# Performance work log

Measured on AMD Instinct MI355X. Metric: run time of the kernel, lower is better.

## Reference

```python
import jax, jax.numpy as jnp
import numpy as np

B, S, EMB, H = 4, 1024, 1024, 16
HD = EMB // H          # head_dim = 64
MAXP = 512             # RelativePositionalEncoder default max_position


def setup_inputs() -> dict:
    key = jax.random.key(0)
    ks = jax.random.split(key, 13)
    s = 1.0 / np.sqrt(EMB)  # xavier-ish scale keeps softmax logits sane
    return {
        "query": jax.random.normal(ks[0], (B, S, EMB), jnp.float32),
        "key": jax.random.normal(ks[1], (B, S, EMB), jnp.float32),
        "value": jax.random.normal(ks[2], (B, S, EMB), jnp.float32),
        "Wq": jax.random.normal(ks[3], (EMB, EMB), jnp.float32) * s,
        "bq": jnp.zeros((EMB,), jnp.float32),
        "Wk": jax.random.normal(ks[4], (EMB, EMB), jnp.float32) * s,
        "bk": jnp.zeros((EMB,), jnp.float32),
        "Wv": jax.random.normal(ks[5], (EMB, EMB), jnp.float32) * s,
        "bv": jnp.zeros((EMB,), jnp.float32),
        "Wo": jax.random.normal(ks[6], (EMB, EMB), jnp.float32) * s,
        "bo": jnp.zeros((EMB,), jnp.float32),
        "rel_k": jax.random.normal(ks[7], (2 * MAXP + 1, HD), jnp.float32) * 0.05,
        "rel_v": jax.random.normal(ks[8], (2 * MAXP + 1, HD), jnp.float32) * 0.05,
    }


def _split_heads(x):
    # [B,S,E] -> [B,S,H,HD] -> [B,H,S,HD] -> [B*H,S,HD]
    return x.reshape(B, S, H, HD).transpose(0, 2, 1, 3).reshape(B * H, S, HD)


def reference(query, key, value, Wq, bq, Wk, bk, Wv, bv, Wo, bo, rel_k, rel_v):
    scale = jnp.sqrt(jnp.asarray(HD, query.dtype))
    q = _split_heads(query @ Wq + bq)
    k = _split_heads(key @ Wk + bk)
    v = _split_heads(value @ Wv + bv)
    # relative position lookup tables: [Sq, Sk, HD]
    rp = jnp.clip(jnp.arange(S)[None, :] - jnp.arange(S)[:, None], -MAXP, MAXP) + MAXP
    a_key = rel_k[rp]
    a_value = rel_v[rp]
    qk = jnp.einsum('bqd,bkd->bqk', q, k)              # [B*H,S,S]
    rel_qk = jnp.einsum('bqd,qkd->bqk', q, a_key)      # relative score term
    attn = jax.nn.softmax((qk + rel_qk) / scale, axis=-1)
    out = jnp.einsum('bqk,bkd->bqd', attn, v) + jnp.einsum('bqk,qkd->bqd', attn, a_value)
    # faithful to original's view(num_heads, batch, -1, head_dim) then concat reshape
    out = out.reshape(H, B, S, HD).transpose(0, 2, 1, 3).reshape(B, S, H * HD)
    out = out @ Wo + bo
    return (out, attn)
```

## Files before the change

### kernel.cpp

```cpp
#include <hip/hip_runtime.h>


using s16x8 = __attribute__((ext_vector_type(8))) short;
using f32x4 = __attribute__((ext_vector_type(4))) float;

#define MFMA16 __builtin_amdgcn_mfma_f32_16x16x32_bf16

__device__ __forceinline__ float bf2f(unsigned short u) {
  union { unsigned int u; float f; } v; v.u = ((unsigned int)u) << 16; return v.f;
}
__device__ __forceinline__ unsigned short f2bf(float f) {
  union { float f; unsigned int u; } v; v.f = f;
  unsigned int r = (v.u + 0x7FFFu + ((v.u >> 16) & 1u)) >> 16;
  return (unsigned short)r;
}

__global__ void k_cvt_bf16(const float* __restrict__ in, unsigned short* __restrict__ out, int n) {
  int i = (blockIdx.x * 256 + threadIdx.x) * 8;
  if (i >= n) return;
  float4 a = *(const float4*)(in + i);
  float4 b = *(const float4*)(in + i + 4);
  s16x8 o;
  o[0] = (short)f2bf(a.x); o[1] = (short)f2bf(a.y); o[2] = (short)f2bf(a.z); o[3] = (short)f2bf(a.w);
  o[4] = (short)f2bf(b.x); o[5] = (short)f2bf(b.y); o[6] = (short)f2bf(b.z); o[7] = (short)f2bf(b.w);
  *(s16x8*)(out + i) = o;
}

__global__ void k_tr1024(const float* __restrict__ W, unsigned short* __restrict__ Wt) {
  __shared__ float t[32][33];
  int tx = threadIdx.x, ty = threadIdx.y;
  int n0 = blockIdx.x * 32, k0 = blockIdx.y * 32;
#pragma unroll
  for (int r = 0; r < 4; ++r)
    t[ty * 4 + r][tx] = W[(size_t)(k0 + ty * 4 + r) * 1024 + n0 + tx];
  __syncthreads();
#pragma unroll
  for (int r = 0; r < 4; ++r)
    Wt[(size_t)(n0 + ty * 4 + r) * 1024 + k0 + tx] = f2bf(t[tx][ty * 4 + r]);
}

__global__ void k_relprep(const float* __restrict__ rk, const float* __restrict__ rv,
                          unsigned short* __restrict__ relkb, unsigned short* __restrict__ rvTb) {
  int b = blockIdx.x;
  if (b < 33) {
    int i = (b * 256 + threadIdx.x) * 8;
    if (i < 65600) {
      float4 a = *(const float4*)(rk + i);
      float4 c = *(const float4*)(rk + i + 4);
      s16x8 o;
      o[0] = (short)f2bf(a.x); o[1] = (short)f2bf(a.y); o[2] = (short)f2bf(a.z); o[3] = (short)f2bf(a.w);
      o[4] = (short)f2bf(c.x); o[5] = (short)f2bf(c.y); o[6] = (short)f2bf(c.z); o[7] = (short)f2bf(c.w);
      *(s16x8*)(relkb + i) = o;
    }
  } else {
    int i = (b - 33) * 256 + threadIdx.x;
    if (i < 65600) {
      int p = i >> 6, d = i & 63;
      rvTb[d * 1040 + p] = f2bf(rv[i]);
    }
  }
}

__global__ __launch_bounds__(256)
void k_trV(const unsigned short* __restrict__ v, unsigned short* __restrict__ vt) {
  __shared__ unsigned short T[64][72];
  const int tid = threadIdx.x;
  const int bh = blockIdx.x >> 4;
  const int s0 = (blockIdx.x & 15) << 6;
  const int r = tid >> 2, cb = (tid & 3) << 4;
  const unsigned short* src = v + ((size_t)bh << 16) + (size_t)(s0 + r) * 64 + cb;
  *(s16x8*)&T[r][cb] = *(const s16x8*)src;
  *(s16x8*)&T[r][cb + 8] = *(const s16x8*)(src + 8);
  __syncthreads();
  unsigned short* dst = vt + ((size_t)bh << 16) + (size_t)r * 1024 + s0 + cb;
  s16x8 o0, o1;
#pragma unroll
  for (int e = 0; e < 8; ++e) o0[e] = T[cb + e][r];
#pragma unroll
  for (int e = 0; e < 8; ++e) o1[e] = T[cb + 8 + e][r];
  *(s16x8*)dst = o0;
  *(s16x8*)(dst + 8) = o1;
}

template <int MODE>
__global__ __launch_bounds__(256, 2)
void k_gemm(const unsigned short* __restrict__ A, const unsigned short* __restrict__ BT,
            const float* __restrict__ bias, void* __restrict__ Cout) {
  __shared__ alignas(16) unsigned short aT[2][4096];
  __shared__ alignas(16) unsigned short bT[2][2048];
  const int tid = threadIdx.x;
  const int lane = tid & 63;
  const int l15 = lane & 15, lhi = lane >> 4;
  const int w = tid >> 6;
  const int wr = w * 32;
  const int brow = blockIdx.y * 128, bcol = blockIdx.x * 64;
  f32x4 acc[2][4] = {};

#define STAGE(buf, kt) do {                                                              \
    int k0s = (kt) * 32;                                                                 \
    {                                                                                    \
      int c = tid;                                                                       \
      int row = c >> 2, k8 = (c & 3) * 8;                                                \
      __builtin_amdgcn_global_load_lds(                                                  \
        (const __attribute__((address_space(1))) void*)(A + (size_t)(brow + row) * 1024 + k0s + k8), \
        (__attribute__((address_space(3))) void*)(&aT[buf][c * 8]), 16, 0, 0);           \
      __builtin_amdgcn_global_load_lds(                                                  \
        (const __attribute__((address_space(1))) void*)(BT + (size_t)(bcol + row) * 1024 + k0s + k8),\
        (__attribute__((address_space(3))) void*)(&bT[buf][c * 8]), 16, 0, 0);           \
    }                                                                                    \
    {                                                                                    \
      int c = tid + 256;                                                                 \
      int row = c >> 2, k8 = (c & 3) * 8;                                                \
      __builtin_amdgcn_global_load_lds(                                                  \
        (const __attribute__((address_space(1))) void*)(A + (size_t)(brow + row) * 1024 + k0s + k8), \
        (__attribute__((address_space(3))) void*)(&aT[buf][c * 8]), 16, 0, 0);           \
    }                                                                                    \
  } while (0)

  int cur = 0;
  STAGE(0, 0);
  for (int kt = 0; kt < 32; ++kt) {
    __syncthreads();
    if (kt + 1 < 32) STAGE(cur ^ 1, kt + 1);
    s16x8 af[2], bfv[4];
#pragma unroll
    for (int m = 0; m < 2; ++m)
      af[m] = *(const s16x8*)&aT[cur][(wr + m * 16 + l15) * 32 + lhi * 8];
#pragma unroll
    for (int n = 0; n < 4; ++n)
      bfv[n] = *(const s16x8*)&bT[cur][(n * 16 + l15) * 32 + lhi * 8];
#pragma unroll
    for (int m = 0; m < 2; ++m)
#pragma unroll
      for (int n = 0; n < 4; ++n)
        acc[m][n] = MFMA16(af[m], bfv[n], acc[m][n], 0, 0, 0);
    __syncthreads();
    cur ^= 1;
  }
#undef STAGE

#pragma unroll
  for (int m = 0; m < 2; ++m) {
#pragma unroll
    for (int n = 0; n < 4; ++n) {
      int col = bcol + n * 16 + l15;
      float bs = bias[col];
#pragma unroll
      for (int j = 0; j < 4; ++j) {
        int r = brow + wr + m * 16 + lhi * 4 + j;
        float v = acc[m][n][j] + bs;
        if (MODE == 0) {
          int b = r >> 10, s = r & 1023, h = col >> 6, d = col & 63;
          ((unsigned short*)Cout)[(((size_t)((b << 4) + h) * 1024 + s) << 6) + d] = f2bf(v);
        } else {
          ((float*)Cout)[(size_t)r * 1024 + col] = v;
        }
      }
    }
  }
}

#define RPW 1032
#define PWP 520

__global__ __launch_bounds__(256, 3)
void k_attn(const unsigned short* __restrict__ qb, const unsigned short* __restrict__ kbm,
            const unsigned short* __restrict__ vT, const unsigned short* __restrict__ relk,
            const unsigned short* __restrict__ rvT, float* __restrict__ attn_out,
            unsigned short* __restrict__ xscr) {
  __shared__ alignas(16) unsigned short pbuf[16 * RPW];
  __shared__ alignas(16) unsigned short pw[16 * PWP];
  __shared__ float red[4][16];
  __shared__ float izS[16], plS[16], phS[16];

  const int tid = threadIdx.x;
  const int lane = tid & 63;
  const int w = tid >> 6;
  const int l15 = lane & 15, lhi = lane >> 4;
  const int orig = ((blockIdx.x & 7) << 9) | (blockIdx.x >> 3);
  const int bh = orig >> 6;
  const int q0 = (orig & 63) << 4;

  const unsigned short* Qh = qb + ((size_t)bh << 16);
  const unsigned short* Kh = kbm + ((size_t)bh << 16);
  const unsigned short* Vth = vT + ((size_t)bh << 16);

  const unsigned short* qp = Qh + (size_t)(q0 + l15) * 64 + lhi * 8;
  s16x8 qa0 = *(const s16x8*)qp;
  s16x8 qa1 = *(const s16x8*)(qp + 32);

  float zp[4] = {0.f, 0.f, 0.f, 0.f};
  for (int k0 = w * 16; k0 < 1024; k0 += 64) {
    const unsigned short* kp = Kh + (size_t)(k0 + l15) * 64 + lhi * 8;
    s16x8 kf0 = *(const s16x8*)kp;
    s16x8 kf1 = *(const s16x8*)(kp + 32);
    const int jb = k0 - q0 - 15;
    int p0 = jb + l15;      p0 = (p0 < -512 ? -512 : (p0 > 512 ? 512 : p0)) + 512;
    int p1 = jb + l15 + 16; p1 = (p1 < -512 ? -512 : (p1 > 512 ? 512 : p1)) + 512;
    const unsigned short* r0p = relk + (size_t)p0 * 64 + lhi * 8;
    const unsigned short* r1p = relk + (size_t)p1 * 64 + lhi * 8;
    s16x8 ra0 = *(const s16x8*)r0p, ra0h = *(const s16x8*)(r0p + 32);
    s16x8 ra1 = *(const s16x8*)r1p, ra1h = *(const s16x8*)(r1p + 32);
    f32x4 c = {0.f, 0.f, 0.f, 0.f};
    f32x4 w0 = {0.f, 0.f, 0.f, 0.f}, w1 = {0.f, 0.f, 0.f, 0.f};
    __builtin_amdgcn_s_setprio(1);
    c = MFMA16(qa0, kf0, c, 0, 0, 0);
    c = MFMA16(qa1, kf1, c, 0, 0, 0);
    w0 = MFMA16(qa0, ra0, w0, 0, 0, 0);  w0 = MFMA16(qa1, ra0h, w0, 0, 0, 0);
    w1 = MFMA16(qa0, ra1, w1, 0, 0, 0);  w1 = MFMA16(qa1, ra1h, w1, 0, 0, 0);
    __builtin_amdgcn_s_setprio(0);
#pragma unroll
    for (int j = 0; j < 4; ++j) {
      int qi = lhi * 4 + j;
      int ts = l15 - qi + 15;
      int sl = (lane & 48) | (ts & 15);
      float a0 = __shfl(w0[j], sl, 64);
      float a1 = __shfl(w1[j], sl, 64);
      float rel = (ts & 16) ? a1 : a0;
      float e = __expf((c[j] + rel) * 0.125f);
      zp[j] += e;
      pbuf[qi * RPW + k0 + l15] = f2bf(e);
    }
  }
#pragma unroll
  for (int off = 1; off < 16; off <<= 1)
#pragma unroll
    for (int j = 0; j < 4; ++j) zp[j] += __shfl_xor(zp[j], off, 64);
  if (l15 == 0) {
#pragma unroll
    for (int j = 0; j < 4; ++j) red[w][lhi * 4 + j] = zp[j];
  }
  __syncthreads();
  if (tid < 16)
    izS[tid] = 1.0f / (red[0][tid] + red[1][tid] + red[2][tid] + red[3][tid]);

  {
    const int qi = tid >> 4, tq = tid & 15;
    const int qa = q0 + qi;
    int lo, hi;
    const bool isPh = (qa < 512);
    if (isPh) { lo = qa + 512; hi = 1024; }
    else      { lo = 0;        hi = qa - 511; }
    float s = 0.f;
    const unsigned short* srow = pbuf + qi * RPW;
    const int kb0 = lo & ~7;
    for (int k8 = kb0 + tq * 8; k8 < hi; k8 += 128) {
      s16x8 v8 = *(const s16x8*)&srow[k8];
#pragma unroll
      for (int e = 0; e < 8; ++e) {
        int k = k8 + e;
        s += (k >= lo && k < hi) ? bf2f((unsigned short)v8[e]) : 0.f;
      }
    }
#pragma unroll
    for (int off = 1; off < 16; off <<= 1) s += __shfl_xor(s, off, 64);
    if (tq == 0) { plS[qi] = isPh ? 0.f : s; phS[qi] = isPh ? s : 0.f; }
  }
  __syncthreads();

  {
    float* ao = attn_out + ((size_t)bh << 20) + ((size_t)q0 << 10);
#pragma unroll
    for (int n = 0; n < 16; ++n) {
      float iz = izS[n];
      union { unsigned int u[2]; } pv;
      *(uint2*)pv.u = *(const uint2*)&pbuf[n * RPW + tid * 4];
      union { unsigned int u; float f; } b0, b1, b2, b3;
      b0.u = pv.u[0] << 16; b1.u = pv.u[0] & 0xFFFF0000u;
      b2.u = pv.u[1] << 16; b3.u = pv.u[1] & 0xFFFF0000u;
      f32x4 o;
      o[0] = b0.f * iz; o[1] = b1.f * iz; o[2] = b2.f * iz; o[3] = b3.f * iz;
      __builtin_nontemporal_store(o, (f32x4*)(ao + (n << 10) + tid * 4));
    }
  }

  f32x4 acc = {0.f, 0.f, 0.f, 0.f};
  const int d0w = w << 4;
  const unsigned short* vrow = Vth + (size_t)(d0w + l15) * 1024 + lhi * 8;
#pragma unroll 8
  for (int kc = 0; kc < 1024; kc += 32) {
    s16x8 pa = *(const s16x8*)&pbuf[l15 * RPW + kc + lhi * 8];
    s16x8 vf = *(const s16x8*)(vrow + kc);
    acc = MFMA16(pa, vf, acc, 0, 0, 0);
  }

  const unsigned short* rrow = rvT + (size_t)(d0w + l15) * 1040 + lhi * 8;
  {
    const int sqi = tid >> 4, stq = tid & 15;
    const int ssh = sqi & 7, shs = ssh >> 1;
    const bool sodd = (ssh & 1) != 0;
    unsigned short* drow = pw + sqi * PWP;
    const unsigned short* srow = pbuf + sqi * RPW;
    for (int ph = 0; ph < 2; ++ph) {
      __syncthreads();
      const int base = q0 + sqi + (ph ? 0 : -512);
      for (int t = stq; t < 64; t += 16) {
        const int kw0 = base + t * 8;
        s16x8 o;
        if (kw0 >= 0 && kw0 + 8 <= 1024) {
          const int A = kw0 - ssh;
          union { s16x8 v; unsigned int u[4]; } a0, a1, ov;
          a0.v = *(const s16x8*)&srow[A];
          a1.v = *(const s16x8*)&srow[A + 8];
          unsigned int wd[8];
#pragma unroll
          for (int j2 = 0; j2 < 4; ++j2) { wd[j2] = a0.u[j2]; wd[4 + j2] = a1.u[j2]; }
          unsigned int v7[7];
#pragma unroll
          for (int j2 = 0; j2 < 7; ++j2) {
            unsigned int sf = (wd[j2] >> 16) | (wd[j2 + 1] << 16);
            v7[j2] = sodd ? sf : wd[j2];
          }
#pragma unroll
          for (int j2 = 0; j2 < 4; ++j2) {
            unsigned int t0 = (shs & 1) ? v7[j2 + 1] : v7[j2];
            unsigned int t1 = (shs & 1) ? v7[j2 + 3] : v7[j2 + 2];
            ov.u[j2] = (shs & 2) ? t1 : t0;
          }
          o = ov.v;
        } else if (kw0 + 8 <= 0 || kw0 >= 1024) {
          o = (s16x8){0, 0, 0, 0, 0, 0, 0, 0};
        } else {
#pragma unroll
          for (int e = 0; e < 8; ++e) {
            int k = kw0 + e;
            int kc2 = k < 0 ? 0 : (k > 1023 ? 1023 : k);
            unsigned short vv = srow[kc2];
            o[e] = (k >= 0 && k < 1024) ? (short)vv : (short)0;
          }
        }
        *(s16x8*)&drow[t * 8] = o;
        if (ph == 0 && t == 0) drow[0] = f2bf(plS[sqi]);
      }
      __syncthreads();
#pragma unroll 8
      for (int kc = 0; kc < 512; kc += 32) {
        s16x8 pa = *(const s16x8*)&pw[l15 * PWP + kc + lhi * 8];
        s16x8 rb = *(const s16x8*)(rrow + (ph << 9) + kc);
        acc = MFMA16(pa, rb, acc, 0, 0, 0);
      }
    }
  }

  float rv1024 = bf2f(rvT[(size_t)(d0w + l15) * 1040 + 1024]);
  const size_t fb = ((size_t)(bh >> 2) << 18) + ((size_t)(bh & 3) << 6);
#pragma unroll
  for (int j = 0; j < 4; ++j) {
    int qi = lhi * 4 + j;
    float v = (acc[j] + phS[qi] * rv1024) * izS[qi];
    xscr[fb + ((size_t)(q0 + qi) << 8) + d0w + l15] = f2bf(v);
  }
}

extern "C" void kernel_launch(void* const* d_in, const int* in_sizes, int n_in,
                              void* d_out, int out_size, void* d_ws, size_t ws_size,
                              hipStream_t stream) {
  (void)in_sizes; (void)n_in; (void)out_size; (void)ws_size;
  const float* query = (const float*)d_in[0];
  const float* key   = (const float*)d_in[1];
  const float* value = (const float*)d_in[2];
  const float* Wq = (const float*)d_in[3];
  const float* bq = (const float*)d_in[4];
  const float* Wk = (const float*)d_in[5];
  const float* bk = (const float*)d_in[6];
  const float* Wv = (const float*)d_in[7];
  const float* bv = (const float*)d_in[8];
  const float* Wo = (const float*)d_in[9];
  const float* bo = (const float*)d_in[10];
  const float* rel_k = (const float*)d_in[11];
  const float* rel_v = (const float*)d_in[12];

  char* ws = (char*)d_ws;
  const size_t MB = 1024 * 1024;
  unsigned short* qb    = (unsigned short*)(ws);
  unsigned short* kbuf  = (unsigned short*)(ws + 8 * MB);
  unsigned short* vbuf  = (unsigned short*)(ws + 16 * MB);
  unsigned short* tmp16 = (unsigned short*)(ws + 24 * MB);
  unsigned short* wt    = (unsigned short*)(ws + 32 * MB);
  unsigned short* relkb = (unsigned short*)(ws + 34 * MB);
  unsigned short* rvTb  = (unsigned short*)(ws + 34 * MB + 512 * 1024);
  unsigned short* vTb   = tmp16;
  unsigned short* xscr  = vbuf;

  float* out0 = (float*)d_out;
  float* attn_out = out0 + 4194304;

  dim3 trb(32, 8), trg(32, 32);
  dim3 gg(16, 32);

  k_relprep<<<290, 256, 0, stream>>>(rel_k, rel_v, relkb, rvTb);

  k_cvt_bf16<<<2048, 256, 0, stream>>>(query, tmp16, 4194304);
  k_tr1024<<<trg, trb, 0, stream>>>(Wq, wt);
  k_gemm<0><<<gg, 256, 0, stream>>>(tmp16, wt, bq, qb);

  k_cvt_bf16<<<2048, 256, 0, stream>>>(key, tmp16, 4194304);
  k_tr1024<<<trg, trb, 0, stream>>>(Wk, wt);
  k_gemm<0><<<gg, 256, 0, stream>>>(tmp16, wt, bk, kbuf);

  k_cvt_bf16<<<2048, 256, 0, stream>>>(value, tmp16, 4194304);
  k_tr1024<<<trg, trb, 0, stream>>>(Wv, wt);
  k_gemm<0><<<gg, 256, 0, stream>>>(tmp16, wt, bv, vbuf);

  k_trV<<<1024, 256, 0, stream>>>(vbuf, vTb);
  k_tr1024<<<trg, trb, 0, stream>>>(Wo, wt);

  k_attn<<<4096, 256, 0, stream>>>(qb, kbuf, vTb, relkb, rvTb, attn_out, xscr);

  k_gemm<1><<<gg, 256, 0, stream>>>(xscr, wt, bo, out0);
}
```

Before: 395.8 us.

## Precompute relative-key score table per block instead of per-tile MFMAs

Replaces the per-key-tile computation of two relative-key MFMA pairs plus shuffles with a per-half precomputed table of q·rel_k values stored in shared memory. Only the unclipped relative positions need MFMAs, and the clipped boundary values are broadcast. The QK MFMA operands are swapped so each lane holds contiguous keys, which lets it pack four bf16 probabilities into one store. The attention write-out is also widened to 16-byte shared loads. This adds extra barriers and table-building passes in exchange for fewer MFMAs and cross-lane shuffles in the score loop.

```diff
diff --git a/kernel.cpp b/kernel.cpp
--- a/kernel.cpp
+++ b/kernel.cpp
@@ -169,9 +169,10 @@
             const unsigned short* __restrict__ rvT, float* __restrict__ attn_out,
             unsigned short* __restrict__ xscr) {
   __shared__ alignas(16) unsigned short pbuf[16 * RPW];
-  __shared__ alignas(16) unsigned short pw[16 * PWP];
+  __shared__ alignas(16) unsigned short TbPw[16 * PWP];
   __shared__ float red[4][16];
   __shared__ float izS[16], plS[16], phS[16];
+  __shared__ unsigned short bndS[32];
 
   const int tid = threadIdx.x;
   const int lane = tid & 63;
@@ -189,47 +190,89 @@
   s16x8 qa0 = *(const s16x8*)qp;
   s16x8 qa1 = *(const s16x8*)(qp + 32);
 
-  float zp[4] = {0.f, 0.f, 0.f, 0.f};
-  for (int k0 = w * 16; k0 < 1024; k0 += 64) {
-    const unsigned short* kp = Kh + (size_t)(k0 + l15) * 64 + lhi * 8;
-    s16x8 kf0 = *(const s16x8*)kp;
-    s16x8 kf1 = *(const s16x8*)(kp + 32);
-    const int jb = k0 - q0 - 15;
-    int p0 = jb + l15;      p0 = (p0 < -512 ? -512 : (p0 > 512 ? 512 : p0)) + 512;
-    int p1 = jb + l15 + 16; p1 = (p1 < -512 ? -512 : (p1 > 512 ? 512 : p1)) + 512;
-    const unsigned short* r0p = relk + (size_t)p0 * 64 + lhi * 8;
-    const unsigned short* r1p = relk + (size_t)p1 * 64 + lhi * 8;
-    s16x8 ra0 = *(const s16x8*)r0p, ra0h = *(const s16x8*)(r0p + 32);
-    s16x8 ra1 = *(const s16x8*)r1p, ra1h = *(const s16x8*)(r1p + 32);
-    f32x4 c = {0.f, 0.f, 0.f, 0.f};
-    f32x4 w0 = {0.f, 0.f, 0.f, 0.f}, w1 = {0.f, 0.f, 0.f, 0.f};
-    __builtin_amdgcn_s_setprio(1);
-    c = MFMA16(qa0, kf0, c, 0, 0, 0);
-    c = MFMA16(qa1, kf1, c, 0, 0, 0);
-    w0 = MFMA16(qa0, ra0, w0, 0, 0, 0);  w0 = MFMA16(qa1, ra0h, w0, 0, 0, 0);
-    w1 = MFMA16(qa0, ra1, w1, 0, 0, 0);  w1 = MFMA16(qa1, ra1h, w1, 0, 0, 0);
-    __builtin_amdgcn_s_setprio(0);
-#pragma unroll
-    for (int j = 0; j < 4; ++j) {
-      int qi = lhi * 4 + j;
-      int ts = l15 - qi + 15;
-      int sl = (lane & 48) | (ts & 15);
-      float a0 = __shfl(w0[j], sl, 64);
-      float a1 = __shfl(w1[j], sl, 64);
-      float rel = (ts & 16) ? a1 : a0;
-      float e = __expf((c[j] + rel) * 0.125f);
-      zp[j] += e;
-      pbuf[qi * RPW + k0 + l15] = f2bf(e);
-    }
-  }
-#pragma unroll
-  for (int off = 1; off < 16; off <<= 1)
-#pragma unroll
-    for (int j = 0; j < 4; ++j) zp[j] += __shfl_xor(zp[j], off, 64);
-  if (l15 == 0) {
-#pragma unroll
-    for (int j = 0; j < 4; ++j) red[w][lhi * 4 + j] = zp[j];
-  }
+  {
+    int sel = (l15 == 1) ? 1024 : 0;
+    const unsigned short* rp = relk + (size_t)sel * 64 + lhi * 8;
+    s16x8 rb0 = *(const s16x8*)rp;
+    s16x8 rb1 = *(const s16x8*)(rp + 32);
+    f32x4 d = {0.f, 0.f, 0.f, 0.f};
+    d = MFMA16(qa0, rb0, d, 0, 0, 0);
+    d = MFMA16(qa1, rb1, d, 0, 0, 0);
+    if (l15 < 2) {
+#pragma unroll
+      for (int j = 0; j < 4; ++j) bndS[l15 * 16 + lhi * 4 + j] = f2bf(d[j]);
+    }
+  }
+
+  float zp = 0.f;
+  for (int half = 0; half < 2; ++half) {
+    const int khalf = half << 9;
+    __syncthreads();
+
+    for (int i = tid; i < 16 * 64; i += 256) {
+      int row = i >> 6, c8 = (i & 63) << 3;
+      int fl = q0 + row - khalf - 512;
+      unsigned short vlo = bndS[row], vhi = bndS[16 + row];
+      s16x8 o;
+#pragma unroll
+      for (int e = 0; e < 8; ++e) o[e] = (short)((c8 + e < fl) ? vlo : vhi);
+      *(s16x8*)&TbPw[row * PWP + c8] = o;
+    }
+    __syncthreads();
+
+    {
+      int pmin = khalf - q0 + 497;
+      int PT0 = (pmin < 0 ? 0 : pmin) & ~15;
+      int PT1 = khalf - q0 + 1023; if (PT1 > 1024) PT1 = 1024;
+      for (int pt = PT0 + w * 16; pt <= PT1; pt += 64) {
+        int pr = pt + l15; if (pr > 1024) pr = 1024;
+        const unsigned short* rp = relk + (size_t)pr * 64 + lhi * 8;
+        s16x8 rf0 = *(const s16x8*)rp;
+        s16x8 rf1 = *(const s16x8*)(rp + 32);
+        f32x4 d = {0.f, 0.f, 0.f, 0.f};
+        d = MFMA16(qa0, rf0, d, 0, 0, 0);
+        d = MFMA16(qa1, rf1, d, 0, 0, 0);
+#pragma unroll
+        for (int j = 0; j < 4; ++j) {
+          int qi = lhi * 4 + j;
+          int p = pt + l15;
+          int u = p - khalf + q0 + qi - 512;
+          if (p <= 1024 && u >= 0 && u < 512) TbPw[qi * PWP + u] = f2bf(d[j]);
+        }
+      }
+    }
+    __syncthreads();
+
+    for (int n = 0; n < 8; ++n) {
+      const int ktile = khalf + w * 16 + n * 64;
+      const unsigned short* kp = Kh + (size_t)(ktile + l15) * 64 + lhi * 8;
+      s16x8 kf0 = *(const s16x8*)kp;
+      s16x8 kf1 = *(const s16x8*)(kp + 32);
+      f32x4 c = {0.f, 0.f, 0.f, 0.f};
+      __builtin_amdgcn_s_setprio(1);
+      c = MFMA16(kf0, qa0, c, 0, 0, 0);
+      c = MFMA16(kf1, qa1, c, 0, 0, 0);
+      __builtin_amdgcn_s_setprio(0);
+      uint2 tv = *(const uint2*)&TbPw[l15 * PWP + (ktile - khalf) + lhi * 4];
+      float t0 = bf2f((unsigned short)(tv.x & 0xFFFF));
+      float t1 = bf2f((unsigned short)(tv.x >> 16));
+      float t2 = bf2f((unsigned short)(tv.y & 0xFFFF));
+      float t3 = bf2f((unsigned short)(tv.y >> 16));
+      float e0 = __expf((c[0] + t0) * 0.125f);
+      float e1 = __expf((c[1] + t1) * 0.125f);
+      float e2 = __expf((c[2] + t2) * 0.125f);
+      float e3 = __expf((c[3] + t3) * 0.125f);
+      zp += (e0 + e1) + (e2 + e3);
+      uint2 pk;
+      pk.x = (unsigned int)f2bf(e0) | ((unsigned int)f2bf(e1) << 16);
+      pk.y = (unsigned int)f2bf(e2) | ((unsigned int)f2bf(e3) << 16);
+      *(uint2*)&pbuf[l15 * RPW + ktile + lhi * 4] = pk;
+    }
+  }
+
+  zp += __shfl_xor(zp, 16, 64);
+  zp += __shfl_xor(zp, 32, 64);
+  if (lane < 16) red[w][lane] = zp;
   __syncthreads();
   if (tid < 16)
     izS[tid] = 1.0f / (red[0][tid] + red[1][tid] + red[2][tid] + red[3][tid]);
@@ -261,16 +304,18 @@
   {
     float* ao = attn_out + ((size_t)bh << 20) + ((size_t)q0 << 10);
 #pragma unroll
-    for (int n = 0; n < 16; ++n) {
-      float iz = izS[n];
-      union { unsigned int u[2]; } pv;
-      *(uint2*)pv.u = *(const uint2*)&pbuf[n * RPW + tid * 4];
-      union { unsigned int u; float f; } b0, b1, b2, b3;
-      b0.u = pv.u[0] << 16; b1.u = pv.u[0] & 0xFFFF0000u;
-      b2.u = pv.u[1] << 16; b3.u = pv.u[1] & 0xFFFF0000u;
-      f32x4 o;
-      o[0] = b0.f * iz; o[1] = b1.f * iz; o[2] = b2.f * iz; o[3] = b3.f * iz;
-      __builtin_nontemporal_store(o, (f32x4*)(ao + (n << 10) + tid * 4));
+    for (int n = 0; n < 8; ++n) {
+      int row = (tid >> 7) + n * 2;
+      int c8 = (tid & 127) << 3;
+      float iz = izS[row];
+      s16x8 p8 = *(const s16x8*)&pbuf[row * RPW + c8];
+      f32x4 o0, o1;
+      o0[0] = bf2f((unsigned short)p8[0]) * iz; o0[1] = bf2f((unsigned short)p8[1]) * iz;
+      o0[2] = bf2f((unsigned short)p8[2]) * iz; o0[3] = bf2f((unsigned short)p8[3]) * iz;
+      o1[0] = bf2f((unsigned short)p8[4]) * iz; o1[1] = bf2f((unsigned short)p8[5]) * iz;
+      o1[2] = bf2f((unsigned short)p8[6]) * iz; o1[3] = bf2f((unsigned short)p8[7]) * iz;
+      __builtin_nontemporal_store(o0, (f32x4*)(ao + (row << 10) + c8));
+      __builtin_nontemporal_store(o1, (f32x4*)(ao + (row << 10) + c8 + 4));
     }
   }
 
@@ -289,7 +334,7 @@
     const int sqi = tid >> 4, stq = tid & 15;
     const int ssh = sqi & 7, shs = ssh >> 1;
     const bool sodd = (ssh & 1) != 0;
-    unsigned short* drow = pw + sqi * PWP;
+    unsigned short* drow = TbPw + sqi * PWP;
     const unsigned short* srow = pbuf + sqi * RPW;
     for (int ph = 0; ph < 2; ++ph) {
       __syncthreads();
@@ -335,7 +380,7 @@
       __syncthreads();
 #pragma unroll 8
       for (int kc = 0; kc < 512; kc += 32) {
-        s16x8 pa = *(const s16x8*)&pw[l15 * PWP + kc + lhi * 8];
+        s16x8 pa = *(const s16x8*)&TbPw[l15 * PWP + kc + lhi * 8];
         s16x8 rb = *(const s16x8*)(rrow + (ph << 9) + kc);
         acc = MFMA16(pa, rb, acc, 0, 0, 0);
       }
```

Result: faster. 368.6 us (-6.9%).
